# Kernel tuning notes

Hardware: AMD Instinct MI355X
Metric: run time of the kernel (lower is better)

## Reference

```python
import jax, jax.numpy as jnp
import numpy as np

NUM_EXPERTS = 8
TOP_K = 2
AUX_COEF = 0.01
B, S, D, H = 4, 2048, 1024, 684


def setup_inputs() -> dict:
    key = jax.random.key(0)
    ks = jax.random.split(key, 5)
    scale_d = 1.0 / np.sqrt(D)
    scale_h = 1.0 / np.sqrt(H)
    return {
        "x": jax.random.normal(ks[0], (B, S, D), dtype=jnp.float32),
        "router_w": jax.random.normal(ks[1], (NUM_EXPERTS, D), dtype=jnp.float32) * scale_d,
        "w1": jax.random.normal(ks[2], (NUM_EXPERTS, H, D), dtype=jnp.float32) * scale_d,
        "w2": jax.random.normal(ks[3], (NUM_EXPERTS, D, H), dtype=jnp.float32) * scale_h,
        "w3": jax.random.normal(ks[4], (NUM_EXPERTS, H, D), dtype=jnp.float32) * scale_d,
    }


def reference(x, router_w, w1, w2, w3):
    b, s, d = x.shape
    xf = x.reshape(-1, d)                                   # [T, d]
    probs = jax.nn.softmax(xf @ router_w.T, axis=-1)        # [T, E]
    topk_probs, topk_idx = jax.lax.top_k(probs, TOP_K)      # [T, k]

    # aux load-balancing loss (uses top-1 assignment density)
    density = jnp.mean(jax.nn.one_hot(topk_idx[:, 0], NUM_EXPERTS, dtype=xf.dtype), axis=0)
    aux_loss = AUX_COEF * jnp.sum(density * probs.mean(axis=0)) * NUM_EXPERTS

    # per-token per-expert combine weight (sums probs if an expert repeats across slots)
    combine = jnp.sum(jax.nn.one_hot(topk_idx, NUM_EXPERTS, dtype=xf.dtype)
                      * topk_probs[..., None], axis=1)      # [T, E]

    out = jnp.zeros_like(xf)
    for e in range(NUM_EXPERTS):  # fixed small expert loop
        h = jax.nn.silu(xf @ w1[e].T) * (xf @ w3[e].T)      # [T, H] SwiGLU
        out = out + combine[:, e:e + 1] * (h @ w2[e].T)     # weighted scatter-combine
    return out.reshape(b, s, d), aux_loss
```

## Files before the change

### kernel.cpp

```cpp
#include <hip/hip_runtime.h>
#include <hip/hip_bf16.h>

#define T_TOK 8192
#define DMODEL 1024
#define HDIM 684
#define HPAD 704
#define NEXP 8

typedef short  bf16x8  __attribute__((ext_vector_type(8)));
typedef float  f32x4   __attribute__((ext_vector_type(4)));

__device__ inline unsigned short f2bu(float f) {
    __hip_bfloat16 h = __float2bfloat16(f);
    return *reinterpret_cast<unsigned short*>(&h);
}

typedef const __attribute__((address_space(1))) unsigned int* gas_p;
typedef __attribute__((address_space(3))) unsigned int* las_p;
__device__ inline void ld_lds16(const unsigned short* g, unsigned short* l) {
    __builtin_amdgcn_global_load_lds((gas_p)g, (las_p)l, 16, 0, 0);
}

#define POS_OFF    74252800ull
#define PAIRS_OFF  74318336ull
#define WS_NEED   141427200ull

__global__ __launch_bounds__(256) void cvt_all(
    const float* __restrict__ w1, const float* __restrict__ w3, const float* __restrict__ w2,
    unsigned short* __restrict__ w1b, unsigned short* __restrict__ w3b,
    unsigned short* __restrict__ w2b, int n4, int n2)
{
    int i = blockIdx.x * 256 + threadIdx.x;
    if (i < 2 * n4) {
        const float* src; unsigned short* dst; int j;
        if (i < n4) { src = w1; dst = w1b; j = i; }
        else        { src = w3; dst = w3b; j = i - n4; }
        float4 v = ((const float4*)src)[j];
        ((ushort4*)dst)[j] = make_ushort4(f2bu(v.x), f2bu(v.y), f2bu(v.z), f2bu(v.w));
        return;
    }
    int j = i - 2 * n4;
    if (j >= n2) return;
    int row = j / 176;
    int col = (j - row * 176) * 4;
    ushort4 o = make_ushort4(0, 0, 0, 0);
    if (col < HDIM) {
        float4 v = *(const float4*)(w2 + (size_t)row * HDIM + col);
        o = make_ushort4(f2bu(v.x), f2bu(v.y), f2bu(v.z), f2bu(v.w));
    }
    *(ushort4*)(w2b + (size_t)row * HPAD + col) = o;
}

__global__ __launch_bounds__(256) void moe_router(
    const float* __restrict__ x, const float* __restrict__ rw,
    unsigned short* __restrict__ xb,
    float* __restrict__ blk_psum, int* __restrict__ blk_t1, int* __restrict__ blk_pc,
    int* __restrict__ topk_idx, float* __restrict__ topk_p)
{
    __shared__ float sp[4][NEXP];
    __shared__ int   si1[4], si2[4];

    int lane = threadIdx.x & 63;
    int w    = threadIdx.x >> 6;
    int t    = blockIdx.x * 4 + w;
    const float* xr = x + (size_t)t * DMODEL;
    unsigned short* xbr = xb + (size_t)t * DMODEL;

    float acc[NEXP];
#pragma unroll
    for (int e = 0; e < NEXP; ++e) acc[e] = 0.f;
#pragma unroll
    for (int j = 0; j < DMODEL / 64; ++j) {
        float xv = xr[j * 64 + lane];
        xbr[j * 64 + lane] = f2bu(xv);
#pragma unroll
        for (int e = 0; e < NEXP; ++e)
            acc[e] += xv * rw[e * DMODEL + j * 64 + lane];
    }
#pragma unroll
    for (int off = 32; off > 0; off >>= 1) {
#pragma unroll
        for (int e = 0; e < NEXP; ++e)
            acc[e] += __shfl_xor(acc[e], off, 64);
    }
    if (lane == 0) {
        float m = acc[0];
#pragma unroll
        for (int e = 1; e < NEXP; ++e) m = fmaxf(m, acc[e]);
        float p[NEXP]; float s = 0.f;
#pragma unroll
        for (int e = 0; e < NEXP; ++e) { p[e] = expf(acc[e] - m); s += p[e]; }
        float inv = 1.f / s;
#pragma unroll
        for (int e = 0; e < NEXP; ++e) p[e] *= inv;
        int i1 = 0;
#pragma unroll
        for (int e = 1; e < NEXP; ++e) if (p[e] > p[i1]) i1 = e;
        int i2 = (i1 == 0) ? 1 : 0;
#pragma unroll
        for (int e = 0; e < NEXP; ++e) if (e != i1 && p[e] > p[i2]) i2 = e;

        topk_idx[t * 2 + 0] = i1;  topk_idx[t * 2 + 1] = i2;
        topk_p[t * 2 + 0] = p[i1]; topk_p[t * 2 + 1] = p[i2];
#pragma unroll
        for (int e = 0; e < NEXP; ++e) sp[w][e] = p[e];
        si1[w] = i1; si2[w] = i2;
    }
    __syncthreads();
    if (threadIdx.x < NEXP) {
        int e = threadIdx.x;
        float ps = sp[0][e] + sp[1][e] + sp[2][e] + sp[3][e];
        int t1 = (si1[0] == e) + (si1[1] == e) + (si1[2] == e) + (si1[3] == e);
        int pc = t1 + (si2[0] == e) + (si2[1] == e) + (si2[2] == e) + (si2[3] == e);
        blk_psum[blockIdx.x * NEXP + e] = ps;
        blk_t1[blockIdx.x * NEXP + e]  = t1;
        blk_pc[blockIdx.x * NEXP + e]  = pc;
    }
}

__global__ __launch_bounds__(256) void moe_scan(
    const float* __restrict__ blk_psum, const int* __restrict__ blk_t1,
    const int* __restrict__ blk_pc,
    int* pair_count, int* offsets, int* cursor, float* aux_out)
{
    __shared__ float wp[4][NEXP];
    __shared__ int   wt[4][NEXP], wc[4][NEXP];
    __shared__ float tp[NEXP];
    __shared__ int   tt1[NEXP], tpc[NEXP];

    int tid = threadIdx.x;
    int lane = tid & 63, w = tid >> 6;
    float lp[NEXP]; int lt[NEXP], lc[NEXP];
#pragma unroll
    for (int e = 0; e < NEXP; ++e) { lp[e] = 0.f; lt[e] = 0; lc[e] = 0; }
    for (int b = tid; b < 2048; b += 256)
#pragma unroll
        for (int e = 0; e < NEXP; ++e) {
            lp[e] += blk_psum[b * NEXP + e];
            lt[e] += blk_t1[b * NEXP + e];
            lc[e] += blk_pc[b * NEXP + e];
        }
#pragma unroll
    for (int off = 32; off > 0; off >>= 1) {
#pragma unroll
        for (int e = 0; e < NEXP; ++e) {
            lp[e] += __shfl_xor(lp[e], off, 64);
            lt[e] += __shfl_xor(lt[e], off, 64);
            lc[e] += __shfl_xor(lc[e], off, 64);
        }
    }
    if (lane == 0) {
#pragma unroll
        for (int e = 0; e < NEXP; ++e) { wp[w][e] = lp[e]; wt[w][e] = lt[e]; wc[w][e] = lc[e]; }
    }
    __syncthreads();
    if (tid < NEXP) {
        int e = tid;
        float s = wp[0][e] + wp[1][e] + wp[2][e] + wp[3][e];
        int t1 = wt[0][e] + wt[1][e] + wt[2][e] + wt[3][e];
        int pc = wc[0][e] + wc[1][e] + wc[2][e] + wc[3][e];
        tp[e] = s; tt1[e] = t1; tpc[e] = pc;
        pair_count[e] = pc;
    }
    __syncthreads();
    if (tid == 0) {
        int run = 0;
        for (int e = 0; e < NEXP; ++e) { offsets[e] = run; cursor[e] = run; run += tpc[e]; }
        float s = 0.f;
        for (int e = 0; e < NEXP; ++e)
            s += ((float)tt1[e] / (float)T_TOK) * (tp[e] / (float)T_TOK);
        aux_out[0] = 0.01f * s * (float)NEXP;
    }
}

__global__ __launch_bounds__(256) void moe_scatter(
    const int* __restrict__ topk_idx, const float* __restrict__ topk_p,
    int* cursor, int* __restrict__ pair_token, float* __restrict__ pair_prob,
    int* __restrict__ pos)
{
    __shared__ int lcnt[NEXP], gbase[NEXP];
    int tid = threadIdx.x;
    if (tid < NEXP) lcnt[tid] = 0;
    __syncthreads();
    int t = blockIdx.x * 256 + tid;
    int e0 = topk_idx[t * 2 + 0], e1 = topk_idx[t * 2 + 1];
    int p0 = atomicAdd(&lcnt[e0], 1);
    int p1 = atomicAdd(&lcnt[e1], 1);
    __syncthreads();
    if (tid < NEXP) gbase[tid] = atomicAdd(&cursor[tid], lcnt[tid]);
    __syncthreads();
    int q0 = gbase[e0] + p0, q1 = gbase[e1] + p1;
    pair_token[q0] = t; pair_prob[q0] = topk_p[t * 2 + 0];
    pair_token[q1] = t; pair_prob[q1] = topk_p[t * 2 + 1];
    pos[t * 2 + 0] = q0; pos[t * 2 + 1] = q1;
}


__global__ __launch_bounds__(512, 4) void moe_ffn1(
    const unsigned short* __restrict__ xb, const unsigned short* __restrict__ w1b,
    const unsigned short* __restrict__ w3b,
    const int* __restrict__ pair_count, const int* __restrict__ offsets,
    const int* __restrict__ pair_token,
    unsigned short* __restrict__ h)
{
    int e   = blockIdx.z;
    int cnt = pair_count[e];
    int m0  = blockIdx.y * 128;
    if (m0 >= cnt) return;
    int base = offsets[e];
    int n0   = blockIdx.x * 128;

    __shared__ unsigned short aT[3 * 4096];
    __shared__ unsigned short b1T[3 * 4096];
    __shared__ unsigned short b3T[3 * 4096];

    int tid  = threadIdx.x;
    int lane = tid & 63, wave = tid >> 6;
    int wm = wave >> 1, wn = wave & 1;

    int srow = lane >> 2;
    int ksg  = (lane & 3) ^ ((lane >> 3) & 3);
    int arow = m0 + wave * 16 + srow; if (arow >= cnt) arow = cnt - 1;
    const unsigned short* ap  = xb + (size_t)pair_token[base + arow] * DMODEL + ksg * 8;
    int brow = n0 + wave * 16 + srow; if (brow > HDIM - 1) brow = HDIM - 1;
    const unsigned short* b1p = w1b + ((size_t)e * HDIM + brow) * DMODEL + ksg * 8;
    const unsigned short* b3p = w3b + ((size_t)e * HDIM + brow) * DMODEL + ksg * 8;
    unsigned short* sA  = aT  + wave * 512;
    unsigned short* sB1 = b1T + wave * 512;
    unsigned short* sB3 = b3T + wave * 512;

    f32x4 acc1[2][4], acc3[2][4];
#pragma unroll
    for (int i = 0; i < 2; ++i)
#pragma unroll
        for (int j = 0; j < 4; ++j) { acc1[i][j] = (f32x4)(0.f); acc3[i][j] = (f32x4)(0.f); }

    int fr  = lane & 15;
    int sz8 = ((lane >> 4) ^ ((fr >> 1) & 3)) * 8;

    ld_lds16(ap,        sA);
    ld_lds16(b1p,       sB1);
    ld_lds16(b3p,       sB3);
    ld_lds16(ap  + 32,  sA  + 4096);
    ld_lds16(b1p + 32,  sB1 + 4096);
    ld_lds16(b3p + 32,  sB3 + 4096);

    const int NIT = DMODEL / 32;
    for (int it = 0; it < NIT; ++it) {
        int buf = it % 3;
        if (it + 1 < NIT) asm volatile("s_waitcnt vmcnt(3)" ::: "memory");
        else              asm volatile("s_waitcnt vmcnt(0)" ::: "memory");
        __builtin_amdgcn_s_barrier();
        asm volatile("" ::: "memory");
        if (it + 2 < NIT) {
            int nb = (it + 2) % 3;
            int nk = (it + 2) * 32;
            ld_lds16(ap  + nk, sA  + nb * 4096);
            ld_lds16(b1p + nk, sB1 + nb * 4096);
            ld_lds16(b3p + nk, sB3 + nb * 4096);
        }
        const unsigned short* cA  = aT  + buf * 4096;
        const unsigned short* cB1 = b1T + buf * 4096;
        const unsigned short* cB3 = b3T + buf * 4096;

        bf16x8 aF[2];
#pragma unroll
        for (int i = 0; i < 2; ++i)
            aF[i] = *(const bf16x8*)&cA[(wm * 32 + i * 16 + fr) * 32 + sz8];
        __builtin_amdgcn_s_setprio(1);
#pragma unroll
        for (int j = 0; j < 4; ++j) {
            int row = (wn * 64 + j * 16 + fr) * 32 + sz8;
            bf16x8 b1F = *(const bf16x8*)&cB1[row];
            bf16x8 b3F = *(const bf16x8*)&cB3[row];
#pragma unroll
            for (int i = 0; i < 2; ++i) {
                acc1[i][j] = __builtin_amdgcn_mfma_f32_16x16x32_bf16(aF[i], b1F, acc1[i][j], 0, 0, 0);
                acc3[i][j] = __builtin_amdgcn_mfma_f32_16x16x32_bf16(aF[i], b3F, acc3[i][j], 0, 0, 0);
            }
        }
        __builtin_amdgcn_s_setprio(0);
    }

    int cbase = n0 + wn * 64 + fr;
    int rbase = m0 + wm * 32 + (lane >> 4) * 4;
#pragma unroll
    for (int i = 0; i < 2; ++i) {
#pragma unroll
        for (int r = 0; r < 4; ++r) {
            int gr = rbase + i * 16 + r;
            if (gr >= cnt) continue;
            unsigned short* hrow = h + (size_t)(base + gr) * HPAD;
#pragma unroll
            for (int j = 0; j < 4; ++j) {
                int col = cbase + j * 16;
                if (col >= HPAD) continue;
                float v1 = acc1[i][j][r];
                float hv = (col < HDIM) ? (v1 / (1.f + expf(-v1))) * acc3[i][j][r] : 0.f;
                hrow[col] = f2bu(hv);
            }
        }
    }
}

__global__ __launch_bounds__(512, 4) void moe_ffn2(
    const unsigned short* __restrict__ h, const unsigned short* __restrict__ w2b,
    const int* __restrict__ pair_count, const int* __restrict__ offsets,
    const int* __restrict__ pair_token, const float* __restrict__ pair_prob,
    float* __restrict__ pairs_out, float* __restrict__ out, int use_atomic)
{
    int e   = blockIdx.z;
    int cnt = pair_count[e];
    int m0  = blockIdx.y * 128;
    if (m0 >= cnt) return;
    int base = offsets[e];
    int n0   = blockIdx.x * 128;

    __shared__ unsigned short aT[3 * 4096];
    __shared__ unsigned short bT[3 * 4096];

    int tid  = threadIdx.x;
    int lane = tid & 63, wave = tid >> 6;
    int wm = wave >> 1, wn = wave & 1;

    int srow = lane >> 2;
    int ksg  = (lane & 3) ^ ((lane >> 3) & 3);
    int arow = m0 + wave * 16 + srow; if (arow >= cnt) arow = cnt - 1;
    const unsigned short* ap = h + (size_t)(base + arow) * HPAD + ksg * 8;
    const unsigned short* bp = w2b + ((size_t)e * DMODEL + n0 + wave * 16 + srow) * HPAD + ksg * 8;
    unsigned short* sA = aT + wave * 512;
    unsigned short* sB = bT + wave * 512;

    f32x4 acc[2][4];
#pragma unroll
    for (int i = 0; i < 2; ++i)
#pragma unroll
        for (int j = 0; j < 4; ++j) acc[i][j] = (f32x4)(0.f);

    int fr  = lane & 15;
    int sz8 = ((lane >> 4) ^ ((fr >> 1) & 3)) * 8;

    ld_lds16(ap,      sA);
    ld_lds16(bp,      sB);
    ld_lds16(ap + 32, sA + 4096);
    ld_lds16(bp + 32, sB + 4096);

    const int NIT = HPAD / 32;
    for (int it = 0; it < NIT; ++it) {
        int buf = it % 3;
        if (it + 1 < NIT) asm volatile("s_waitcnt vmcnt(2)" ::: "memory");
        else              asm volatile("s_waitcnt vmcnt(0)" ::: "memory");
        __builtin_amdgcn_s_barrier();
        asm volatile("" ::: "memory");
        if (it + 2 < NIT) {
            int nb = (it + 2) % 3;
            int nk = (it + 2) * 32;
            ld_lds16(ap + nk, sA + nb * 4096);
            ld_lds16(bp + nk, sB + nb * 4096);
        }
        const unsigned short* cA = aT + buf * 4096;
        const unsigned short* cB = bT + buf * 4096;

        bf16x8 aF[2];
#pragma unroll
        for (int i = 0; i < 2; ++i)
            aF[i] = *(const bf16x8*)&cA[(wm * 32 + i * 16 + fr) * 32 + sz8];
        __builtin_amdgcn_s_setprio(1);
#pragma unroll
        for (int j = 0; j < 4; ++j) {
            bf16x8 bF = *(const bf16x8*)&cB[(wn * 64 + j * 16 + fr) * 32 + sz8];
#pragma unroll
            for (int i = 0; i < 2; ++i)
                acc[i][j] = __builtin_amdgcn_mfma_f32_16x16x32_bf16(aF[i], bF, acc[i][j], 0, 0, 0);
        }
        __builtin_amdgcn_s_setprio(0);
    }

    int cbase = n0 + wn * 64 + fr;
    int rbase = m0 + wm * 32 + (lane >> 4) * 4;
#pragma unroll
    for (int i = 0; i < 2; ++i) {
#pragma unroll
        for (int r = 0; r < 4; ++r) {
            int gr = rbase + i * 16 + r;
            if (gr >= cnt) continue;
            int gp = base + gr;
            float pw = pair_prob[gp];
            if (!use_atomic) {
                float* prow = pairs_out + (size_t)gp * DMODEL;
#pragma unroll
                for (int j = 0; j < 4; ++j)
                    prow[cbase + j * 16] = pw * acc[i][j][r];
            } else {
                float* orow = out + (size_t)pair_token[gp] * DMODEL;
#pragma unroll
                for (int j = 0; j < 4; ++j)
                    atomicAdd(&orow[cbase + j * 16], pw * acc[i][j][r]);
            }
        }
    }
}

__global__ __launch_bounds__(256) void moe_combine(
    const float* __restrict__ pairs_out, const int* __restrict__ pos,
    float* __restrict__ out)
{
    int t = blockIdx.x;
    int c = threadIdx.x;
    int q0 = pos[t * 2 + 0], q1 = pos[t * 2 + 1];
    float4 a = ((const float4*)(pairs_out + (size_t)q0 * DMODEL))[c];
    float4 b = ((const float4*)(pairs_out + (size_t)q1 * DMODEL))[c];
    float4 o;
    o.x = a.x + b.x; o.y = a.y + b.y; o.z = a.z + b.z; o.w = a.w + b.w;
    ((float4*)(out + (size_t)t * DMODEL))[c] = o;
}

extern "C" void kernel_launch(void* const* d_in, const int* in_sizes, int n_in,
                              void* d_out, int out_size, void* d_ws, size_t ws_size,
                              hipStream_t stream)
{
    const float* x  = (const float*)d_in[0];
    const float* rw = (const float*)d_in[1];
    const float* w1 = (const float*)d_in[2];
    const float* w2 = (const float*)d_in[3];
    const float* w3 = (const float*)d_in[4];
    float* out = (float*)d_out;

    char* ws = (char*)d_ws;
    int*   pair_count = (int*)(ws + 0);
    int*   offsets    = (int*)(ws + 32);
    int*   cursor     = (int*)(ws + 64);
    float* blk_psum   = (float*)(ws + 256);
    int*   blk_t1     = (int*)(ws + 65792);
    int*   blk_pc     = (int*)(ws + 131328);
    int*   topk_idx   = (int*)(ws + 196864);
    float* topk_p     = (float*)(ws + 262400);
    int*   pair_token = (int*)(ws + 327936);
    float* pair_prob  = (float*)(ws + 393472);
    unsigned short* xb  = (unsigned short*)(ws + 459264);
    unsigned short* w1b = (unsigned short*)(ws + 17236480);
    unsigned short* w3b = (unsigned short*)(ws + 28443136);
    unsigned short* w2b = (unsigned short*)(ws + 39649792);
    unsigned short* hbuf= (unsigned short*)(ws + 51184128);
    int*   pos        = (int*)(ws + POS_OFF);
    float* pairs_out  = (float*)(ws + PAIRS_OFF);

    int two_pass = (ws_size >= WS_NEED) ? 1 : 0;
    if (!two_pass)
        hipMemsetAsync(d_out, 0, (size_t)out_size * sizeof(float), stream);

    int n4 = NEXP * HDIM * DMODEL / 4;
    int n2 = NEXP * DMODEL * (HPAD / 4);
    cvt_all<<<(2 * n4 + n2 + 255) / 256, 256, 0, stream>>>(w1, w3, w2, w1b, w3b, w2b, n4, n2);

    moe_router <<<T_TOK / 4, 256, 0, stream>>>(x, rw, xb, blk_psum, blk_t1, blk_pc, topk_idx, topk_p);
    moe_scan   <<<1, 256, 0, stream>>>(blk_psum, blk_t1, blk_pc, pair_count, offsets, cursor,
                                       out + (size_t)T_TOK * DMODEL);
    moe_scatter<<<T_TOK / 256, 256, 0, stream>>>(topk_idx, topk_p, cursor, pair_token, pair_prob, pos);

    moe_ffn1<<<dim3(6, 64, 8), 512, 0, stream>>>(xb, w1b, w3b, pair_count, offsets, pair_token, hbuf);
    moe_ffn2<<<dim3(8, 64, 8), 512, 0, stream>>>(hbuf, w2b, pair_count, offsets, pair_token, pair_prob,
                                                 pairs_out, out, two_pass ? 0 : 1);
    if (two_pass)
        moe_combine<<<T_TOK, 256, 0, stream>>>(pairs_out, pos, out);
}
```

Measured before the change: 302.9 us.

## Use 4-wave blocks with larger per-wave MFMA tiles in expert FFN kernels

Both expert GEMM kernels drop from 8 waves to 4 waves per block, and each wave now computes a larger tile. In ffn1 each wave covers 64x64 for both w1 and w3; in ffn2 each wave covers 64x128 and the block N tile widens to 256. The larger tiles increase register-level reuse of the A and B fragments loaded from LDS and cut barrier overhead per MFMA. The cost is much higher accumulator register pressure and fewer waves per CU for hiding latency, and ffn2 launches fewer blocks.

```diff
diff --git a/kernel.cpp b/kernel.cpp
--- a/kernel.cpp
+++ b/kernel.cpp
@@ -196,7 +196,7 @@
 }
 
 
-__global__ __launch_bounds__(512, 4) void moe_ffn1(
+__global__ __launch_bounds__(256, 2) void moe_ffn1(
     const unsigned short* __restrict__ xb, const unsigned short* __restrict__ w1b,
     const unsigned short* __restrict__ w3b,
     const int* __restrict__ pair_count, const int* __restrict__ offsets,
@@ -220,53 +220,56 @@
 
     int srow = lane >> 2;
     int ksg  = (lane & 3) ^ ((lane >> 3) & 3);
-    int arow = m0 + wave * 16 + srow; if (arow >= cnt) arow = cnt - 1;
-    const unsigned short* ap  = xb + (size_t)pair_token[base + arow] * DMODEL + ksg * 8;
-    int brow = n0 + wave * 16 + srow; if (brow > HDIM - 1) brow = HDIM - 1;
-    const unsigned short* b1p = w1b + ((size_t)e * HDIM + brow) * DMODEL + ksg * 8;
-    const unsigned short* b3p = w3b + ((size_t)e * HDIM + brow) * DMODEL + ksg * 8;
-    unsigned short* sA  = aT  + wave * 512;
-    unsigned short* sB1 = b1T + wave * 512;
-    unsigned short* sB3 = b3T + wave * 512;
-
-    f32x4 acc1[2][4], acc3[2][4];
-#pragma unroll
-    for (int i = 0; i < 2; ++i)
+    int ar0 = m0 + wave * 16 + srow;      if (ar0 >= cnt) ar0 = cnt - 1;
+    int ar1 = m0 + 64 + wave * 16 + srow; if (ar1 >= cnt) ar1 = cnt - 1;
+    const unsigned short* ap0 = xb + (size_t)pair_token[base + ar0] * DMODEL + ksg * 8;
+    const unsigned short* ap1 = xb + (size_t)pair_token[base + ar1] * DMODEL + ksg * 8;
+    int br0 = n0 + wave * 16 + srow;      if (br0 > HDIM - 1) br0 = HDIM - 1;
+    int br1 = n0 + 64 + wave * 16 + srow; if (br1 > HDIM - 1) br1 = HDIM - 1;
+    const unsigned short* b1p0 = w1b + ((size_t)e * HDIM + br0) * DMODEL + ksg * 8;
+    const unsigned short* b1p1 = w1b + ((size_t)e * HDIM + br1) * DMODEL + ksg * 8;
+    const unsigned short* b3p0 = w3b + ((size_t)e * HDIM + br0) * DMODEL + ksg * 8;
+    const unsigned short* b3p1 = w3b + ((size_t)e * HDIM + br1) * DMODEL + ksg * 8;
+    int wof0 = wave * 512, wof1 = 2048 + wave * 512;
+
+#define STAGE_F1(bf, koff) do { \
+    ld_lds16(ap0  + (koff), aT  + (bf) * 4096 + wof0); \
+    ld_lds16(ap1  + (koff), aT  + (bf) * 4096 + wof1); \
+    ld_lds16(b1p0 + (koff), b1T + (bf) * 4096 + wof0); \
+    ld_lds16(b1p1 + (koff), b1T + (bf) * 4096 + wof1); \
+    ld_lds16(b3p0 + (koff), b3T + (bf) * 4096 + wof0); \
+    ld_lds16(b3p1 + (koff), b3T + (bf) * 4096 + wof1); \
+  } while (0)
+
+    f32x4 acc1[4][4], acc3[4][4];
+#pragma unroll
+    for (int i = 0; i < 4; ++i)
 #pragma unroll
         for (int j = 0; j < 4; ++j) { acc1[i][j] = (f32x4)(0.f); acc3[i][j] = (f32x4)(0.f); }
 
     int fr  = lane & 15;
     int sz8 = ((lane >> 4) ^ ((fr >> 1) & 3)) * 8;
 
-    ld_lds16(ap,        sA);
-    ld_lds16(b1p,       sB1);
-    ld_lds16(b3p,       sB3);
-    ld_lds16(ap  + 32,  sA  + 4096);
-    ld_lds16(b1p + 32,  sB1 + 4096);
-    ld_lds16(b3p + 32,  sB3 + 4096);
+    STAGE_F1(0, 0);
+    STAGE_F1(1, 32);
 
     const int NIT = DMODEL / 32;
     for (int it = 0; it < NIT; ++it) {
         int buf = it % 3;
-        if (it + 1 < NIT) asm volatile("s_waitcnt vmcnt(3)" ::: "memory");
+        if (it + 1 < NIT) asm volatile("s_waitcnt vmcnt(6)" ::: "memory");
         else              asm volatile("s_waitcnt vmcnt(0)" ::: "memory");
         __builtin_amdgcn_s_barrier();
         asm volatile("" ::: "memory");
-        if (it + 2 < NIT) {
-            int nb = (it + 2) % 3;
-            int nk = (it + 2) * 32;
-            ld_lds16(ap  + nk, sA  + nb * 4096);
-            ld_lds16(b1p + nk, sB1 + nb * 4096);
-            ld_lds16(b3p + nk, sB3 + nb * 4096);
-        }
+        if (it + 2 < NIT) STAGE_F1((it + 2) % 3, (it + 2) * 32);
+
         const unsigned short* cA  = aT  + buf * 4096;
         const unsigned short* cB1 = b1T + buf * 4096;
         const unsigned short* cB3 = b3T + buf * 4096;
 
-        bf16x8 aF[2];
-#pragma unroll
-        for (int i = 0; i < 2; ++i)
-            aF[i] = *(const bf16x8*)&cA[(wm * 32 + i * 16 + fr) * 32 + sz8];
+        bf16x8 aF[4];
+#pragma unroll
+        for (int i = 0; i < 4; ++i)
+            aF[i] = *(const bf16x8*)&cA[(wm * 64 + i * 16 + fr) * 32 + sz8];
         __builtin_amdgcn_s_setprio(1);
 #pragma unroll
         for (int j = 0; j < 4; ++j) {
@@ -274,18 +277,19 @@
             bf16x8 b1F = *(const bf16x8*)&cB1[row];
             bf16x8 b3F = *(const bf16x8*)&cB3[row];
 #pragma unroll
-            for (int i = 0; i < 2; ++i) {
+            for (int i = 0; i < 4; ++i) {
                 acc1[i][j] = __builtin_amdgcn_mfma_f32_16x16x32_bf16(aF[i], b1F, acc1[i][j], 0, 0, 0);
                 acc3[i][j] = __builtin_amdgcn_mfma_f32_16x16x32_bf16(aF[i], b3F, acc3[i][j], 0, 0, 0);
             }
         }
         __builtin_amdgcn_s_setprio(0);
     }
+#undef STAGE_F1
 
     int cbase = n0 + wn * 64 + fr;
-    int rbase = m0 + wm * 32 + (lane >> 4) * 4;
-#pragma unroll
-    for (int i = 0; i < 2; ++i) {
+    int rbase = m0 + wm * 64 + (lane >> 4) * 4;
+#pragma unroll
+    for (int i = 0; i < 4; ++i) {
 #pragma unroll
         for (int r = 0; r < 4; ++r) {
             int gr = rbase + i * 16 + r;
@@ -303,7 +307,7 @@
     }
 }
 
-__global__ __launch_bounds__(512, 4) void moe_ffn2(
+__global__ __launch_bounds__(256, 2) void moe_ffn2(
     const unsigned short* __restrict__ h, const unsigned short* __restrict__ w2b,
     const int* __restrict__ pair_count, const int* __restrict__ offsets,
     const int* __restrict__ pair_token, const float* __restrict__ pair_prob,
@@ -314,10 +318,10 @@
     int m0  = blockIdx.y * 128;
     if (m0 >= cnt) return;
     int base = offsets[e];
-    int n0   = blockIdx.x * 128;
+    int n0   = blockIdx.x * 256;
 
     __shared__ unsigned short aT[3 * 4096];
-    __shared__ unsigned short bT[3 * 4096];
+    __shared__ unsigned short bT[3 * 8192];
 
     int tid  = threadIdx.x;
     int lane = tid & 63, wave = tid >> 6;
@@ -325,61 +329,70 @@
 
     int srow = lane >> 2;
     int ksg  = (lane & 3) ^ ((lane >> 3) & 3);
-    int arow = m0 + wave * 16 + srow; if (arow >= cnt) arow = cnt - 1;
-    const unsigned short* ap = h + (size_t)(base + arow) * HPAD + ksg * 8;
-    const unsigned short* bp = w2b + ((size_t)e * DMODEL + n0 + wave * 16 + srow) * HPAD + ksg * 8;
-    unsigned short* sA = aT + wave * 512;
-    unsigned short* sB = bT + wave * 512;
-
-    f32x4 acc[2][4];
-#pragma unroll
-    for (int i = 0; i < 2; ++i)
-#pragma unroll
-        for (int j = 0; j < 4; ++j) acc[i][j] = (f32x4)(0.f);
+    int ar0 = m0 + wave * 16 + srow;      if (ar0 >= cnt) ar0 = cnt - 1;
+    int ar1 = m0 + 64 + wave * 16 + srow; if (ar1 >= cnt) ar1 = cnt - 1;
+    const unsigned short* ap0 = h + (size_t)(base + ar0) * HPAD + ksg * 8;
+    const unsigned short* ap1 = h + (size_t)(base + ar1) * HPAD + ksg * 8;
+    int brr = n0 + wave * 16 + srow;
+    const unsigned short* bp0 = w2b + ((size_t)e * DMODEL + brr)       * HPAD + ksg * 8;
+    const unsigned short* bp1 = w2b + ((size_t)e * DMODEL + brr + 64)  * HPAD + ksg * 8;
+    const unsigned short* bp2 = w2b + ((size_t)e * DMODEL + brr + 128) * HPAD + ksg * 8;
+    const unsigned short* bp3 = w2b + ((size_t)e * DMODEL + brr + 192) * HPAD + ksg * 8;
+    int wof = wave * 512;
+
+#define STAGE_F2(bf, koff) do { \
+    ld_lds16(ap0 + (koff), aT + (bf) * 4096 + wof); \
+    ld_lds16(ap1 + (koff), aT + (bf) * 4096 + wof + 2048); \
+    ld_lds16(bp0 + (koff), bT + (bf) * 8192 + wof); \
+    ld_lds16(bp1 + (koff), bT + (bf) * 8192 + wof + 2048); \
+    ld_lds16(bp2 + (koff), bT + (bf) * 8192 + wof + 4096); \
+    ld_lds16(bp3 + (koff), bT + (bf) * 8192 + wof + 6144); \
+  } while (0)
+
+    f32x4 acc[4][8];
+#pragma unroll
+    for (int i = 0; i < 4; ++i)
+#pragma unroll
+        for (int j = 0; j < 8; ++j) acc[i][j] = (f32x4)(0.f);
 
     int fr  = lane & 15;
     int sz8 = ((lane >> 4) ^ ((fr >> 1) & 3)) * 8;
 
-    ld_lds16(ap,      sA);
-    ld_lds16(bp,      sB);
-    ld_lds16(ap + 32, sA + 4096);
-    ld_lds16(bp + 32, sB + 4096);
+    STAGE_F2(0, 0);
+    STAGE_F2(1, 32);
 
     const int NIT = HPAD / 32;
     for (int it = 0; it < NIT; ++it) {
         int buf = it % 3;
-        if (it + 1 < NIT) asm volatile("s_waitcnt vmcnt(2)" ::: "memory");
+        if (it + 1 < NIT) asm volatile("s_waitcnt vmcnt(6)" ::: "memory");
         else              asm volatile("s_waitcnt vmcnt(0)" ::: "memory");
         __builtin_amdgcn_s_barrier();
         asm volatile("" ::: "memory");
-        if (it + 2 < NIT) {
-            int nb = (it + 2) % 3;
-            int nk = (it + 2) * 32;
-            ld_lds16(ap + nk, sA + nb * 4096);
-            ld_lds16(bp + nk, sB + nb * 4096);
-        }
+        if (it + 2 < NIT) STAGE_F2((it + 2) % 3, (it + 2) * 32);
+
         const unsigned short* cA = aT + buf * 4096;
-        const unsigned short* cB = bT + buf * 4096;
-
-        bf16x8 aF[2];
-#pragma unroll
-        for (int i = 0; i < 2; ++i)
-            aF[i] = *(const bf16x8*)&cA[(wm * 32 + i * 16 + fr) * 32 + sz8];
+        const unsigned short* cB = bT + buf * 8192;
+
+        bf16x8 aF[4];
+#pragma unroll
+        for (int i = 0; i < 4; ++i)
+            aF[i] = *(const bf16x8*)&cA[(wm * 64 + i * 16 + fr) * 32 + sz8];
         __builtin_amdgcn_s_setprio(1);
 #pragma unroll
-        for (int j = 0; j < 4; ++j) {
-            bf16x8 bF = *(const bf16x8*)&cB[(wn * 64 + j * 16 + fr) * 32 + sz8];
-#pragma unroll
-            for (int i = 0; i < 2; ++i)
+        for (int j = 0; j < 8; ++j) {
+            bf16x8 bF = *(const bf16x8*)&cB[(wn * 128 + j * 16 + fr) * 32 + sz8];
+#pragma unroll
+            for (int i = 0; i < 4; ++i)
                 acc[i][j] = __builtin_amdgcn_mfma_f32_16x16x32_bf16(aF[i], bF, acc[i][j], 0, 0, 0);
         }
         __builtin_amdgcn_s_setprio(0);
     }
-
-    int cbase = n0 + wn * 64 + fr;
-    int rbase = m0 + wm * 32 + (lane >> 4) * 4;
-#pragma unroll
-    for (int i = 0; i < 2; ++i) {
+#undef STAGE_F2
+
+    int cbase = n0 + wn * 128 + fr;
+    int rbase = m0 + wm * 64 + (lane >> 4) * 4;
+#pragma unroll
+    for (int i = 0; i < 4; ++i) {
 #pragma unroll
         for (int r = 0; r < 4; ++r) {
             int gr = rbase + i * 16 + r;
@@ -389,12 +402,12 @@
             if (!use_atomic) {
                 float* prow = pairs_out + (size_t)gp * DMODEL;
 #pragma unroll
-                for (int j = 0; j < 4; ++j)
+                for (int j = 0; j < 8; ++j)
                     prow[cbase + j * 16] = pw * acc[i][j][r];
             } else {
                 float* orow = out + (size_t)pair_token[gp] * DMODEL;
 #pragma unroll
-                for (int j = 0; j < 4; ++j)
+                for (int j = 0; j < 8; ++j)
                     atomicAdd(&orow[cbase + j * 16], pw * acc[i][j][r]);
             }
         }
@@ -458,8 +471,8 @@
                                        out + (size_t)T_TOK * DMODEL);
     moe_scatter<<<T_TOK / 256, 256, 0, stream>>>(topk_idx, topk_p, cursor, pair_token, pair_prob, pos);
 
-    moe_ffn1<<<dim3(6, 64, 8), 512, 0, stream>>>(xb, w1b, w3b, pair_count, offsets, pair_token, hbuf);
-    moe_ffn2<<<dim3(8, 64, 8), 512, 0, stream>>>(hbuf, w2b, pair_count, offsets, pair_token, pair_prob,
+    moe_ffn1<<<dim3(6, 64, 8), 256, 0, stream>>>(xb, w1b, w3b, pair_count, offsets, pair_token, hbuf);
+    moe_ffn2<<<dim3(4, 64, 8), 256, 0, stream>>>(hbuf, w2b, pair_count, offsets, pair_token, pair_prob,
                                                  pairs_out, out, two_pass ? 0 : 1);
     if (two_pass)
         moe_combine<<<T_TOK, 256, 0, stream>>>(pairs_out, pos, out);
```

New measurement: 320.0 us. +5.7%, slower.
